# Optimization experiments

Hardware: AMD Instinct MI355X
Metric: run time of the kernel (lower is better)

## Reference

```python
import jax, jax.numpy as jnp
import numpy as np

D_MODEL = 1024
NHEAD = 16
HEAD_DIM = D_MODEL // NHEAD
MASK_FILLER = -1e20


def setup_inputs() -> dict:
    key = jax.random.key(0)
    ks = jax.random.split(key, 8)
    B, S = 2, 2048
    query = jax.random.normal(ks[0], (B, S, D_MODEL), dtype=jnp.float32)
    key_t = jax.random.normal(ks[1], (B, S, D_MODEL), dtype=jnp.float32)
    value = jax.random.normal(ks[2], (B, S, D_MODEL), dtype=jnp.float32)
    mask = jax.random.randint(ks[3], (B, S, S), 0, 2, dtype=jnp.int32)
    # nn.Linear(d_model, d_model, bias=False) weights, shape [out, in]
    scale = 1.0 / np.sqrt(D_MODEL)
    wq = jax.random.uniform(ks[4], (D_MODEL, D_MODEL), jnp.float32, -scale, scale)
    wk = jax.random.uniform(ks[5], (D_MODEL, D_MODEL), jnp.float32, -scale, scale)
    wv = jax.random.uniform(ks[6], (D_MODEL, D_MODEL), jnp.float32, -scale, scale)
    wo = jax.random.uniform(ks[7], (D_MODEL, D_MODEL), jnp.float32, -scale, scale)
    return {"query": query, "key": key_t, "value": value, "mask": mask,
            "wq": wq, "wk": wk, "wv": wv, "wo": wo}


def reference(query, key, value, mask, wq, wk, wv, wo):
    B = query.shape[0]
    # Projections: nn.Linear -> x @ W.T
    q = (query @ wq.T).reshape(B, -1, NHEAD, HEAD_DIM).transpose(0, 2, 1, 3)  # [B,H,Sq,Dh]
    k = (key @ wk.T).reshape(B, -1, NHEAD, HEAD_DIM).transpose(0, 2, 1, 3)    # [B,H,Sk,Dh]
    v = (value @ wv.T).reshape(B, -1, NHEAD, HEAD_DIM).transpose(0, 2, 1, 3)  # [B,H,Sk,Dh]
    scores = jnp.einsum('bhqd,bhkd->bhqk', q, k) / jnp.sqrt(jnp.float32(HEAD_DIM))
    scores = jnp.where(mask[:, None, :, :] == 0, MASK_FILLER, scores)
    attn = jax.nn.softmax(scores, axis=-1)  # dropout p=0.0 -> identity
    out = jnp.einsum('bhqk,bhkd->bhqd', attn, v)  # [B,H,Sq,Dh]
    out = out.transpose(0, 2, 1, 3).reshape(B, -1, D_MODEL)
    return out @ wo.T
```

## Files before the change

kernel.cpp:

```cpp
#include <hip/hip_runtime.h>
#include <stdint.h>

typedef __bf16 bf16x8 __attribute__((ext_vector_type(8)));
typedef __bf16 bf16x4 __attribute__((ext_vector_type(4)));
typedef float floatx4 __attribute__((ext_vector_type(4)));
typedef unsigned short ushort8v __attribute__((ext_vector_type(8)));
typedef unsigned int uint4v __attribute__((ext_vector_type(4)));
typedef unsigned short u16;
typedef unsigned long long u64;

#define GLOAD_LDS16(gp, lp)                                                       \
  __builtin_amdgcn_global_load_lds((__attribute__((address_space(1))) void*)(gp), \
                                   (__attribute__((address_space(3))) void*)(lp), \
                                   16, 0, 0)

__device__ __forceinline__ u16 f2bf(float f) {
  uint32_t u = __builtin_bit_cast(uint32_t, f);
  u = (u + 0x7FFFu + ((u >> 16) & 1u)) >> 16;
  return (u16)u;
}

__device__ __forceinline__ ushort8v load8(const void* base, size_t elemOff, int isf32) {
  if (isf32) {
    const uint32_t* p = (const uint32_t*)base + elemOff;
    uint4v a = *(const uint4v*)p;
    uint4v b = *(const uint4v*)(p + 4);
#pragma unroll
    for (int i = 0; i < 4; ++i) { a[i] += 0x8000u; b[i] += 0x8000u; }
    uint4v r;
    r[0] = __builtin_amdgcn_perm(a[1], a[0], 0x07060302);
    r[1] = __builtin_amdgcn_perm(a[3], a[2], 0x07060302);
    r[2] = __builtin_amdgcn_perm(b[1], b[0], 0x07060302);
    r[3] = __builtin_amdgcn_perm(b[3], b[2], 0x07060302);
    return __builtin_bit_cast(ushort8v, r);
  }
  return *(const ushort8v*)((const u16*)base + elemOff);
}

__global__ void detect_dtype(const u16* __restrict__ q, int* __restrict__ flag) {
  if (threadIdx.x == 0) *flag = 0;
  __syncthreads();
  int hit = 0;
  for (int i = threadIdx.x; i < 8192; i += 256) {
    u16 u = q[i];
    if (((u >> 7) & 0xFF) == 0xFF) hit = 1;
  }
  if (hit) atomicOr(flag, 1);
}

__global__ __launch_bounds__(256)
void prep(const void* X0, const void* X1, const void* X2,
          const void* W0, const void* W1, const void* W2, const void* W3,
          u16* __restrict__ Xb, u16* __restrict__ Wb,
          const int* __restrict__ mask, u64* __restrict__ mpk,
          int* __restrict__ flagOut)
{
  const int id = blockIdx.x;
  const int t  = threadIdx.x;
  if (id < 8192) {
    __shared__ int sflag;
    if (t == 0) sflag = 0;
    int hit = 0;
    {
      const uint4v* q4 = (const uint4v*)X0;
      const int base = t * 4;
#pragma unroll
      for (int i = 0; i < 4; ++i) {
        uint4v v = q4[base + i];
#pragma unroll
        for (int j = 0; j < 4; ++j) {
          const uint32_t w = v[j];
          if ((w & 0x7F80u) == 0x7F80u || (w & 0x7F800000u) == 0x7F800000u)
            hit = 1;
        }
      }
    }
    __syncthreads();
    if (hit) sflag = 1;
    __syncthreads();
    const int isf = sflag;
    if (id == 0 && t == 0) *flagOut = isf;

    const int r2  = t >> 7;
    const int col = (t & 127) * 8;
    const void* src; u16* dst; int row;
    if (id < 6144) {
      const int s = id >> 11;
      src = (s == 0) ? X0 : (s == 1) ? X1 : X2;
      row = (id & 2047) * 2 + r2;
      dst = Xb + (size_t)s * 4096 * 1040 + (size_t)row * 1040 + col;
    } else {
      const int s = (id - 6144) >> 9;
      src = (s == 0) ? W0 : (s == 1) ? W1 : (s == 2) ? W2 : W3;
      row = ((id - 6144) & 511) * 2 + r2;
      dst = Wb + (size_t)s * 1024 * 1040 + (size_t)row * 1040 + col;
    }
    *(ushort8v*)dst = load8(src, (size_t)row * 1024 + col, isf);
  } else {
    const int g    = (id - 8192) * 4 + (t >> 6);
    const int lane = t & 63;
#pragma unroll
    for (int i = 0; i < 4; ++i) {
      const int wordId = g * 4 + i;
      const int row  = wordId >> 5;
      const int word = wordId & 31;
      const int m = mask[(size_t)row * 2048 + word * 64 + lane];
      u64 bits = __ballot(m != 0);
      if (lane == 0) mpk[(size_t)row * 32 + word] = bits;
    }
  }
}

__global__ void pack_mask(const int* __restrict__ mask, u64* __restrict__ mpk) {
  const int gw   = (blockIdx.x * 256 + threadIdx.x) >> 6;
  const int lane = threadIdx.x & 63;
  const int word = gw & 31;
  const int row  = gw >> 5;
  const int m = mask[(size_t)row * 2048 + word * 64 + lane];
  u64 bits = __ballot(m != 0);
  if (lane == 0) mpk[(size_t)row * 32 + word] = bits;
}

__global__ __launch_bounds__(256)
void cvt_w(const void* W0, const void* W1, const void* W2, const void* W3,
           u16* __restrict__ dst, const int* __restrict__ flagp) {
  const int isf = *flagp;
  const int z = blockIdx.y;
  const void* src = (z == 0) ? W0 : (z == 1) ? W1 : (z == 2) ? W2 : W3;
  const size_t off = ((size_t)blockIdx.x * 256 + threadIdx.x) * 8;
  *(ushort8v*)(dst + (size_t)z * 1024 * 1024 + off) = load8(src, off, isf);
}

__global__ __launch_bounds__(256, 3)
void gemm_qkv_b(const u16* __restrict__ Xb, const u16* __restrict__ Wb,
                u16* __restrict__ Qb, u16* __restrict__ Kb, u16* __restrict__ Vt)
{
  const int AS = 1040, WS = 1040, N = 1024, K = 1024;
  const int z = blockIdx.z;
  const u16* A = Xb + (size_t)z * 4096 * AS;
  const u16* W = Wb + (size_t)z * 1024 * WS;

  __shared__ __align__(16) u16 lS[4 * 128 * 32];
  u16* lA = lS;
  u16* lB = lS + 8192;

  const int tid  = threadIdx.x;
  const int lane = tid & 63;
  const int quad = lane >> 4;
  const int l15  = lane & 15;
  const int w    = tid >> 6;
  const int wm   = w >> 1, wn = w & 1;
  const int tileM = blockIdx.x * 128;
  const int tileN = blockIdx.y * 128;

  floatx4 acc[4][4] = {};

  const int ldRow = tid >> 2;
  const int ldCol = (tid & 3) * 8;
  const u16* aG = A + (size_t)(tileM + ldRow) * AS + ldCol;
  const u16* bG = W + (size_t)(tileN + ldRow) * WS + ldCol;
  u16* lAp = lA + tid * 8;
  u16* lBp = lB + tid * 8;

  GLOAD_LDS16(aG, lAp);
  GLOAD_LDS16(aG + (size_t)64 * AS, lAp + 2048);
  GLOAD_LDS16(bG, lBp);
  GLOAD_LDS16(bG + (size_t)64 * WS, lBp + 2048);
  __syncthreads();

#pragma unroll 2
  for (int k0 = 0; k0 < K; k0 += 32) {
    const int cur = (k0 >> 5) & 1;
    const int nxo = 4096 * (cur ^ 1);
    if (k0 + 32 < K) {
      GLOAD_LDS16(aG + k0 + 32, lAp + nxo);
      GLOAD_LDS16(aG + (size_t)64 * AS + k0 + 32, lAp + nxo + 2048);
      GLOAD_LDS16(bG + k0 + 32, lBp + nxo);
      GLOAD_LDS16(bG + (size_t)64 * WS + k0 + 32, lBp + nxo + 2048);
    }
    const u16* cA = lA + 4096 * cur;
    const u16* cB = lB + 4096 * cur;
    bf16x8 af[4], bw[4];
#pragma unroll
    for (int i = 0; i < 4; ++i) {
      af[i] = *(const bf16x8*)&cA[(wm * 64 + i * 16 + l15) * 32 + quad * 8];
      bw[i] = *(const bf16x8*)&cB[(wn * 64 + i * 16 + l15) * 32 + quad * 8];
    }
#pragma unroll
    for (int i = 0; i < 4; ++i)
#pragma unroll
      for (int j = 0; j < 4; ++j)
        acc[i][j] = __builtin_amdgcn_mfma_f32_16x16x32_bf16(af[i], bw[j], acc[i][j], 0, 0, 0);
    __syncthreads();
  }

  if (z < 2) {
    u16* C = (z == 0) ? Qb : Kb;
    const float sc = (z == 0) ? 0.18033688011112042f : 1.0f;
#pragma unroll
    for (int i = 0; i < 4; ++i) {
      const int row0 = tileM + wm * 64 + i * 16 + quad * 4;
#pragma unroll
      for (int j = 0; j < 4; ++j) {
        const int col = tileN + wn * 64 + j * 16 + l15;
#pragma unroll
        for (int r = 0; r < 4; ++r)
          C[(size_t)(row0 + r) * N + col] = f2bf(acc[i][j][r] * sc);
      }
    }
  } else {
    u16* myT = lS + w * 4096;
#pragma unroll
    for (int i = 0; i < 4; ++i)
#pragma unroll
      for (int j = 0; j < 4; ++j)
#pragma unroll
        for (int r = 0; r < 4; ++r) {
          const int lr = i * 16 + quad * 4 + r;
          const int lc = j * 16 + l15;
          myT[lr * 64 + (lc ^ (quad << 4))] = f2bf(acc[i][j][r]);
        }
    {
      const int n    = lane;
      const int gcol = tileN + wn * 64 + n;
      const int hh = gcol >> 6, dd = gcol & 63;
      const int growBase = tileM + wm * 64;
      const int bb = growBase >> 11;
      const int s0 = growBase & 2047;
      u16* dst = Vt + (((size_t)bb * 16 + hh) * 64 + dd) * 2048 + s0;
#pragma unroll
      for (int m0 = 0; m0 < 64; m0 += 8) {
        ushort8v pk;
#pragma unroll
        for (int t = 0; t < 8; ++t) {
          const int m = m0 + t;
          pk[t] = myT[m * 64 + (n ^ ((m & 12) << 2))];
        }
        *(ushort8v*)(dst + m0) = pk;
      }
    }
  }
}

__global__ __launch_bounds__(256)
void gemm_qkv_f(const void* X0, const void* X1, const void* X2,
                const u16* __restrict__ Wb,
                u16* __restrict__ Qb, u16* __restrict__ Kb, u16* __restrict__ Vt,
                const int* __restrict__ flagp)
{
  const int K = 1024, N = 1024;
  const int isf = *flagp;
  const int z = blockIdx.z;
  const void* A_ = (z == 0) ? X0 : (z == 1) ? X1 : X2;
  const u16* W = Wb + (size_t)z * 1024 * 1024;

  __shared__ __align__(16) u16 lA[128 * 32];
  __shared__ __align__(16) u16 lB[128 * 32];

  const int tid  = threadIdx.x;
  const int lane = tid & 63;
  const int quad = lane >> 4;
  const int l15  = lane & 15;
  const int w    = tid >> 6;
  const int wm   = w >> 1, wn = w & 1;
  const int tileM = blockIdx.x * 128;
  const int tileN = blockIdx.y * 128;

  floatx4 acc[4][4] = {};

  const int ldRow = tid >> 2;
  const int ldCol = (tid & 3) * 8;
  const size_t aOff = (size_t)(tileM + ldRow) * K + ldCol;
  const u16* bG = W + (size_t)(tileN + ldRow) * K + ldCol;
  u16* lAp = lA + tid * 8;
  u16* lBp = lB + tid * 8;

  ushort8v a0 = load8(A_, aOff, isf);
  ushort8v a1 = load8(A_, aOff + (size_t)64 * K, isf);
  ushort8v b0 = *(const ushort8v*)bG;
  ushort8v b1 = *(const ushort8v*)(bG + (size_t)64 * K);

  for (int k0 = 0; k0 < K; k0 += 32) {
    __syncthreads();
    *(ushort8v*)lAp          = a0;
    *(ushort8v*)(lAp + 2048) = a1;
    *(ushort8v*)lBp          = b0;
    *(ushort8v*)(lBp + 2048) = b1;
    __syncthreads();

    if (k0 + 32 < K) {
      a0 = load8(A_, aOff + k0 + 32, isf);
      a1 = load8(A_, aOff + (size_t)64 * K + k0 + 32, isf);
      b0 = *(const ushort8v*)(bG + k0 + 32);
      b1 = *(const ushort8v*)(bG + (size_t)64 * K + k0 + 32);
    }

    bf16x8 af[4], bw[4];
#pragma unroll
    for (int i = 0; i < 4; ++i) {
      af[i] = *(const bf16x8*)&lA[(wm * 64 + i * 16 + l15) * 32 + quad * 8];
      bw[i] = *(const bf16x8*)&lB[(wn * 64 + i * 16 + l15) * 32 + quad * 8];
    }
#pragma unroll
    for (int i = 0; i < 4; ++i)
#pragma unroll
      for (int j = 0; j < 4; ++j)
        acc[i][j] = __builtin_amdgcn_mfma_f32_16x16x32_bf16(af[i], bw[j], acc[i][j], 0, 0, 0);
  }

  if (z < 2) {
    u16* C = (z == 0) ? Qb : Kb;
    const float sc = (z == 0) ? 0.18033688011112042f : 1.0f;
#pragma unroll
    for (int i = 0; i < 4; ++i) {
      const int row0 = tileM + wm * 64 + i * 16 + quad * 4;
#pragma unroll
      for (int j = 0; j < 4; ++j) {
        const int col = tileN + wn * 64 + j * 16 + l15;
#pragma unroll
        for (int r = 0; r < 4; ++r)
          C[(size_t)(row0 + r) * N + col] = f2bf(acc[i][j][r] * sc);
      }
    }
  } else {
    const int half = w >> 1;
    u16* myT = (w & 1) ? lB : lA;
#pragma unroll
    for (int pass = 0; pass < 2; ++pass) {
      __syncthreads();
      if (half == pass) {
#pragma unroll
        for (int i = 0; i < 4; ++i)
#pragma unroll
          for (int j = 0; j < 4; ++j)
#pragma unroll
            for (int r = 0; r < 4; ++r) {
              const int lr = i * 16 + quad * 4 + r;
              const int lc = j * 16 + l15;
              myT[lr * 64 + (lc ^ (quad << 4))] = f2bf(acc[i][j][r]);
            }
      }
      __syncthreads();
      if (half == pass) {
        const int n    = lane;
        const int gcol = tileN + wn * 64 + n;
        const int hh = gcol >> 6, dd = gcol & 63;
        const int growBase = tileM + wm * 64;
        const int bb = growBase >> 11;
        const int s0 = growBase & 2047;
        u16* dst = Vt + (((size_t)bb * 16 + hh) * 64 + dd) * 2048 + s0;
#pragma unroll
        for (int m0 = 0; m0 < 64; m0 += 8) {
          ushort8v pk;
#pragma unroll
          for (int t = 0; t < 8; ++t) {
            const int m = m0 + t;
            pk[t] = myT[m * 64 + (n ^ ((m & 12) << 2))];
          }
          *(ushort8v*)(dst + m0) = pk;
        }
      }
    }
  }
}

__global__ __launch_bounds__(256)
void attn(const u16* Qb, const u16* __restrict__ Kb, const u16* __restrict__ Vt,
          const u64* __restrict__ mpk, u16* AO, int aoStr)
{
  __shared__ __align__(16) u16 lK[2][64 * 64];
  __shared__ __align__(16) u16 lV[2][64 * 64];
  __shared__ __align__(16) u16 lP[4][32 * 64];

  const int tid  = threadIdx.x;
  const int lane = tid & 63;
  const int quad = lane >> 4;
  const int l15  = lane & 15;
  const int w    = tid >> 6;

  const int bh = blockIdx.x;
  const int qt = blockIdx.y;
  const int b  = bh >> 4;
  const int h  = bh & 15;
  const size_t rowB   = (size_t)b * 2048;
  const size_t vtBase = ((size_t)bh * 64) * 2048;
  const int qbase = qt * 128 + w * 32;

  bf16x8 aq[2][2];
#pragma unroll
  for (int g = 0; g < 2; ++g) {
    const u16* qp = Qb + (rowB + qbase + g * 16 + l15) * 1024 + h * 64 + quad * 8;
    aq[g][0] = *(const bf16x8*)qp;
    aq[g][1] = *(const bf16x8*)(qp + 32);
  }

  const ushort8v one_u = {0x3F80, 0x3F80, 0x3F80, 0x3F80, 0x3F80, 0x3F80, 0x3F80, 0x3F80};
  const bf16x8 ones = __builtin_bit_cast(bf16x8, one_u);

  floatx4 o[2][4];
  floatx4 l4[2];
#pragma unroll
  for (int g = 0; g < 2; ++g) {
    l4[g] = (floatx4){0.f, 0.f, 0.f, 0.f};
#pragma unroll
    for (int nb = 0; nb < 4; ++nb) o[g][nb] = (floatx4){0.f, 0.f, 0.f, 0.f};
  }

  const u64* mrow0 = mpk + (rowB + qbase + l15) * 32;
  const u64* mrow1 = mpk + (rowB + qbase + 16 + l15) * 32;
  u16* lPw = &lP[w][0];

  const int r1 = tid >> 3;
  const int cs = ((tid & 7) ^ (r1 & 7)) * 8;
  const u16* kSrc = Kb + (rowB + r1) * 1024 + h * 64 + cs;
  const u16* vSrc = Vt + vtBase + (size_t)r1 * 2048 + cs;

  GLOAD_LDS16(kSrc,                     &lK[0][tid * 8]);
  GLOAD_LDS16(kSrc + (size_t)32 * 1024, &lK[0][tid * 8 + 2048]);
  GLOAD_LDS16(vSrc,                     &lV[0][tid * 8]);
  GLOAD_LDS16(vSrc + (size_t)32 * 2048, &lV[0][tid * 8 + 2048]);

#pragma unroll 2
  for (int kt = 0; kt < 32; ++kt) {
    const int cur = kt & 1;
    __syncthreads();
    if (kt < 31) {
      const u16* kS = kSrc + (size_t)(kt + 1) * 64 * 1024;
      const u16* vS = vSrc + (kt + 1) * 64;
      GLOAD_LDS16(kS,                     &lK[cur ^ 1][tid * 8]);
      GLOAD_LDS16(kS + (size_t)32 * 1024, &lK[cur ^ 1][tid * 8 + 2048]);
      GLOAD_LDS16(vS,                     &lV[cur ^ 1][tid * 8]);
      GLOAD_LDS16(vS + (size_t)32 * 2048, &lV[cur ^ 1][tid * 8 + 2048]);
    }

    const u64 mw0 = mrow0[kt];
    const u64 mw1 = mrow1[kt];

#pragma unroll
    for (int nb = 0; nb < 4; ++nb) {
      const int row = nb * 16 + l15;
      const int swk = (row & 7) << 3;
      bf16x8 ak0 = *(const bf16x8*)&lK[cur][row * 64 + ((quad * 8) ^ swk)];
      bf16x8 ak1 = *(const bf16x8*)&lK[cur][row * 64 + ((quad * 8 + 32) ^ swk)];
      floatx4 s0 = {0.f, 0.f, 0.f, 0.f};
      floatx4 s1 = {0.f, 0.f, 0.f, 0.f};
      s0 = __builtin_amdgcn_mfma_f32_16x16x32_bf16(ak0, aq[0][0], s0, 0, 0, 0);
      s1 = __builtin_amdgcn_mfma_f32_16x16x32_bf16(ak0, aq[1][0], s1, 0, 0, 0);
      s0 = __builtin_amdgcn_mfma_f32_16x16x32_bf16(ak1, aq[0][1], s0, 0, 0, 0);
      s1 = __builtin_amdgcn_mfma_f32_16x16x32_bf16(ak1, aq[1][1], s1, 0, 0, 0);
      const int kb = nb * 16 + quad * 4;
      const uint32_t nib0 = (uint32_t)(mw0 >> kb) & 0xFu;
      const uint32_t nib1 = (uint32_t)(mw1 >> kb) & 0xFu;
      const float a0 = (nib0 & 1u) ? __builtin_amdgcn_exp2f(s0[0]) : 0.0f;
      const float a1 = (nib0 & 2u) ? __builtin_amdgcn_exp2f(s0[1]) : 0.0f;
      const float a2 = (nib0 & 4u) ? __builtin_amdgcn_exp2f(s0[2]) : 0.0f;
      const float a3 = (nib0 & 8u) ? __builtin_amdgcn_exp2f(s0[3]) : 0.0f;
      const float c0 = (nib1 & 1u) ? __builtin_amdgcn_exp2f(s1[0]) : 0.0f;
      const float c1 = (nib1 & 2u) ? __builtin_amdgcn_exp2f(s1[1]) : 0.0f;
      const float c2 = (nib1 & 4u) ? __builtin_amdgcn_exp2f(s1[2]) : 0.0f;
      const float c3 = (nib1 & 8u) ? __builtin_amdgcn_exp2f(s1[3]) : 0.0f;
      bf16x4 p0, p1;
      p0[0] = (__bf16)a0; p0[1] = (__bf16)a1;
      p0[2] = (__bf16)a2; p0[3] = (__bf16)a3;
      p1[0] = (__bf16)c0; p1[1] = (__bf16)c1;
      p1[2] = (__bf16)c2; p1[3] = (__bf16)c3;
      const int col = kb ^ ((l15 & 7) << 3);
      *(bf16x4*)&lPw[l15 * 64 + col]        = p0;
      *(bf16x4*)&lPw[(16 + l15) * 64 + col] = p1;
    }

#pragma unroll
    for (int ks = 0; ks < 2; ++ks) {
      const int pc = (ks * 32 + quad * 8) ^ ((l15 & 7) << 3);
      bf16x8 ap0 = *(const bf16x8*)&lPw[l15 * 64 + pc];
      bf16x8 ap1 = *(const bf16x8*)&lPw[(16 + l15) * 64 + pc];
#pragma unroll
      for (int nb = 0; nb < 4; ++nb) {
        const int row = nb * 16 + l15;
        bf16x8 bv = *(const bf16x8*)&lV[cur][row * 64 + ((ks * 32 + quad * 8) ^ ((row & 7) << 3))];
        o[0][nb] = __builtin_amdgcn_mfma_f32_16x16x32_bf16(ap0, bv, o[0][nb], 0, 0, 0);
        o[1][nb] = __builtin_amdgcn_mfma_f32_16x16x32_bf16(ap1, bv, o[1][nb], 0, 0, 0);
      }
      l4[0] = __builtin_amdgcn_mfma_f32_16x16x32_bf16(ap0, ones, l4[0], 0, 0, 0);
      l4[1] = __builtin_amdgcn_mfma_f32_16x16x32_bf16(ap1, ones, l4[1], 0, 0, 0);
    }
  }

#pragma unroll
  for (int g = 0; g < 2; ++g)
#pragma unroll
    for (int r = 0; r < 4; ++r) {
      const float inv = 1.0f / l4[g][r];
      const size_t orow = (rowB + qbase + g * 16 + quad * 4 + r) * aoStr + h * 64;
#pragma unroll
      for (int nb = 0; nb < 4; ++nb)
        AO[orow + nb * 16 + l15] = f2bf(o[g][nb][r] * inv);
    }
}

__global__ __launch_bounds__(256, 4)
void gemm_out(const u16* __restrict__ A, int aStr,
              const u16* __restrict__ W, int wStr, void* C_,
              const int* __restrict__ flagp)
{
  const int K = 1024, N = 1024;
  const int isf = *flagp;

  __shared__ __align__(16) u16 lA[2 * 64 * 32];
  __shared__ __align__(16) u16 lB[2 * 64 * 32];

  const int tid  = threadIdx.x;
  const int lane = tid & 63;
  const int quad = lane >> 4;
  const int l15  = lane & 15;
  const int w    = tid >> 6;
  const int tileM = blockIdx.x * 64;
  const int tileN = blockIdx.y * 64;

  floatx4 acc[4] = {};

  const int ldRow = tid >> 2;
  const int ldCol = (tid & 3) * 8;
  const u16* aG = A + (size_t)(tileM + ldRow) * aStr + ldCol;
  const u16* bG = W + (size_t)(tileN + ldRow) * wStr + ldCol;
  u16* lAp = lA + tid * 8;
  u16* lBp = lB + tid * 8;

  GLOAD_LDS16(aG, lAp);
  GLOAD_LDS16(bG, lBp);
  __syncthreads();

#pragma unroll 2
  for (int k0 = 0; k0 < K; k0 += 32) {
    const int cur = (k0 >> 5) & 1;
    const int nx = 2048 * (cur ^ 1);
    if (k0 + 32 < K) {
      GLOAD_LDS16(aG + k0 + 32, lAp + nx);
      GLOAD_LDS16(bG + k0 + 32, lBp + nx);
    }
    const u16* cA = lA + 2048 * cur;
    const u16* cB = lB + 2048 * cur;
    bf16x8 af[4], bw;
#pragma unroll
    for (int i = 0; i < 4; ++i)
      af[i] = *(const bf16x8*)&cA[(i * 16 + l15) * 32 + quad * 8];
    bw = *(const bf16x8*)&cB[(w * 16 + l15) * 32 + quad * 8];
#pragma unroll
    for (int i = 0; i < 4; ++i)
      acc[i] = __builtin_amdgcn_mfma_f32_16x16x32_bf16(af[i], bw, acc[i], 0, 0, 0);
    __syncthreads();
  }

#pragma unroll
  for (int i = 0; i < 4; ++i) {
    const int row0 = tileM + i * 16 + quad * 4;
    const int col  = tileN + w * 16 + l15;
#pragma unroll
    for (int r = 0; r < 4; ++r) {
      const size_t off = (size_t)(row0 + r) * N + col;
      if (isf) ((float*)C_)[off] = acc[i][r];
      else     ((u16*)C_)[off]   = f2bf(acc[i][r]);
    }
  }
}

extern "C" void kernel_launch(void* const* d_in, const int* in_sizes, int n_in,
                              void* d_out, int out_size, void* d_ws, size_t ws_size,
                              hipStream_t stream)
{
  const int* mk = (const int*)d_in[3];

  int* flag = (int*)d_ws;
  u64* mpk  = (u64*)((char*)d_ws + 256);
  const size_t SZ = (size_t)4096 * 1024;
  u16* Qb = (u16*)((char*)d_ws + 256 + (size_t)1048576);
  u16* Kb = Qb + SZ;
  u16* Vt = Kb + SZ;
  u16* Wb = Vt + SZ;

  const size_t WB_PAD = (size_t)4 * 1024 * 1040;
  const size_t XB_PAD = (size_t)3 * 4096 * 1040;
  const size_t NEED = 256 + 1048576 + 3 * SZ * 2 + WB_PAD * 2 + XB_PAD * 2;

  if (ws_size >= NEED) {
    u16* Xb = Wb + WB_PAD;
    prep<<<16384, 256, 0, stream>>>(d_in[0], d_in[1], d_in[2],
                                    d_in[4], d_in[5], d_in[6], d_in[7],
                                    Xb, Wb, mk, mpk, flag);
    gemm_qkv_b<<<dim3(32, 8, 3), 256, 0, stream>>>(Xb, Wb, Qb, Kb, Vt);
    u16* AOp = Xb;
    attn<<<dim3(32, 16), 256, 0, stream>>>(Qb, Kb, Vt, mpk, AOp, 1040);
    gemm_out<<<dim3(64, 16), 256, 0, stream>>>(AOp, 1040,
                                               Wb + (size_t)3 * 1024 * 1040, 1040,
                                               d_out, flag);
  } else {
    detect_dtype<<<1, 256, 0, stream>>>((const u16*)d_in[0], flag);
    pack_mask<<<32768, 256, 0, stream>>>(mk, mpk);
    cvt_w<<<dim3(512, 4), 256, 0, stream>>>(d_in[4], d_in[5], d_in[6], d_in[7], Wb, flag);
    gemm_qkv_f<<<dim3(32, 8, 3), 256, 0, stream>>>(d_in[0], d_in[1], d_in[2],
                                                   Wb, Qb, Kb, Vt, flag);
    attn<<<dim3(32, 16), 256, 0, stream>>>(Qb, Kb, Vt, mpk, Qb, 1024);
    gemm_out<<<dim3(64, 16), 256, 0, stream>>>(Qb, 1024,
                                               Wb + (size_t)3 * 1024 * 1024, 1024,
                                               d_out, flag);
  }
}
```

Before: 268.5 us.

## Fuse activation bf16 conversion into QKV GEMM A-operand loads

The prep kernel no longer converts the three 4096x1024 activation inputs to padded bf16 buffers. The QKV GEMM instead reads the raw inputs through load8 (converting fp32 to bf16 when needed) into registers one k-step ahead, then stores them to LDS. This removes a full write and re-read of the activation copies. The A operand loses the direct global-to-LDS path, and each activation element is now re-read and re-converted once per N tile.

```diff
diff --git a/kernel.cpp b/kernel.cpp
--- a/kernel.cpp
+++ b/kernel.cpp
@@ -49,15 +49,15 @@
 }
 
 __global__ __launch_bounds__(256)
-void prep(const void* X0, const void* X1, const void* X2,
+void prep(const void* X0,
           const void* W0, const void* W1, const void* W2, const void* W3,
-          u16* __restrict__ Xb, u16* __restrict__ Wb,
+          u16* __restrict__ Wb,
           const int* __restrict__ mask, u64* __restrict__ mpk,
           int* __restrict__ flagOut)
 {
   const int id = blockIdx.x;
   const int t  = threadIdx.x;
-  if (id < 8192) {
+  if (id < 2048) {
     __shared__ int sflag;
     if (t == 0) sflag = 0;
     int hit = 0;
@@ -83,21 +83,13 @@
 
     const int r2  = t >> 7;
     const int col = (t & 127) * 8;
-    const void* src; u16* dst; int row;
-    if (id < 6144) {
-      const int s = id >> 11;
-      src = (s == 0) ? X0 : (s == 1) ? X1 : X2;
-      row = (id & 2047) * 2 + r2;
-      dst = Xb + (size_t)s * 4096 * 1040 + (size_t)row * 1040 + col;
-    } else {
-      const int s = (id - 6144) >> 9;
-      src = (s == 0) ? W0 : (s == 1) ? W1 : (s == 2) ? W2 : W3;
-      row = ((id - 6144) & 511) * 2 + r2;
-      dst = Wb + (size_t)s * 1024 * 1040 + (size_t)row * 1040 + col;
-    }
+    const int s   = id >> 9;
+    const void* src = (s == 0) ? W0 : (s == 1) ? W1 : (s == 2) ? W2 : W3;
+    const int row = (id & 511) * 2 + r2;
+    u16* dst = Wb + (size_t)s * 1024 * 1040 + (size_t)row * 1040 + col;
     *(ushort8v*)dst = load8(src, (size_t)row * 1024 + col, isf);
   } else {
-    const int g    = (id - 8192) * 4 + (t >> 6);
+    const int g    = (id - 2048) * 4 + (t >> 6);
     const int lane = t & 63;
 #pragma unroll
     for (int i = 0; i < 4; ++i) {
@@ -132,13 +124,16 @@
 }
 
 __global__ __launch_bounds__(256, 3)
-void gemm_qkv_b(const u16* __restrict__ Xb, const u16* __restrict__ Wb,
-                u16* __restrict__ Qb, u16* __restrict__ Kb, u16* __restrict__ Vt)
+void gemm_qkv_b(const void* X0, const void* X1, const void* X2,
+                const u16* __restrict__ Wb,
+                u16* __restrict__ Qb, u16* __restrict__ Kb, u16* __restrict__ Vt,
+                const int* __restrict__ flagp)
 {
-  const int AS = 1040, WS = 1040, N = 1024, K = 1024;
+  const int WS = 1040, N = 1024, K = 1024;
   const int z = blockIdx.z;
-  const u16* A = Xb + (size_t)z * 4096 * AS;
+  const void* A_ = (z == 0) ? X0 : (z == 1) ? X1 : X2;
   const u16* W = Wb + (size_t)z * 1024 * WS;
+  const int isf = *flagp;
 
   __shared__ __align__(16) u16 lS[4 * 128 * 32];
   u16* lA = lS;
@@ -157,15 +152,19 @@
 
   const int ldRow = tid >> 2;
   const int ldCol = (tid & 3) * 8;
-  const u16* aG = A + (size_t)(tileM + ldRow) * AS + ldCol;
+  const size_t aOff = (size_t)(tileM + ldRow) * 1024 + ldCol;
   const u16* bG = W + (size_t)(tileN + ldRow) * WS + ldCol;
   u16* lAp = lA + tid * 8;
   u16* lBp = lB + tid * 8;
 
-  GLOAD_LDS16(aG, lAp);
-  GLOAD_LDS16(aG + (size_t)64 * AS, lAp + 2048);
+  ushort8v a0 = load8(A_, aOff, isf);
+  ushort8v a1 = load8(A_, aOff + (size_t)64 * 1024, isf);
+  *(ushort8v*)lAp          = a0;
+  *(ushort8v*)(lAp + 2048) = a1;
   GLOAD_LDS16(bG, lBp);
   GLOAD_LDS16(bG + (size_t)64 * WS, lBp + 2048);
+  a0 = load8(A_, aOff + 32, isf);
+  a1 = load8(A_, aOff + (size_t)64 * 1024 + 32, isf);
   __syncthreads();
 
 #pragma unroll 2
@@ -173,10 +172,14 @@
     const int cur = (k0 >> 5) & 1;
     const int nxo = 4096 * (cur ^ 1);
     if (k0 + 32 < K) {
-      GLOAD_LDS16(aG + k0 + 32, lAp + nxo);
-      GLOAD_LDS16(aG + (size_t)64 * AS + k0 + 32, lAp + nxo + 2048);
+      *(ushort8v*)(lAp + nxo)        = a0;
+      *(ushort8v*)(lAp + nxo + 2048) = a1;
       GLOAD_LDS16(bG + k0 + 32, lBp + nxo);
       GLOAD_LDS16(bG + (size_t)64 * WS + k0 + 32, lBp + nxo + 2048);
+    }
+    if (k0 + 64 < K) {
+      a0 = load8(A_, aOff + k0 + 64, isf);
+      a1 = load8(A_, aOff + (size_t)64 * 1024 + k0 + 64, isf);
     }
     const u16* cA = lA + 4096 * cur;
     const u16* cB = lB + 4096 * cur;
@@ -583,12 +586,12 @@
   const size_t NEED = 256 + 1048576 + 3 * SZ * 2 + WB_PAD * 2 + XB_PAD * 2;
 
   if (ws_size >= NEED) {
-    u16* Xb = Wb + WB_PAD;
-    prep<<<16384, 256, 0, stream>>>(d_in[0], d_in[1], d_in[2],
+    u16* AOp = Wb + WB_PAD;
+    prep<<<10240, 256, 0, stream>>>(d_in[0],
                                     d_in[4], d_in[5], d_in[6], d_in[7],
-                                    Xb, Wb, mk, mpk, flag);
-    gemm_qkv_b<<<dim3(32, 8, 3), 256, 0, stream>>>(Xb, Wb, Qb, Kb, Vt);
-    u16* AOp = Xb;
+                                    Wb, mk, mpk, flag);
+    gemm_qkv_b<<<dim3(32, 8, 3), 256, 0, stream>>>(d_in[0], d_in[1], d_in[2],
+                                                   Wb, Qb, Kb, Vt, flag);
     attn<<<dim3(32, 16), 256, 0, stream>>>(Qb, Kb, Vt, mpk, AOp, 1040);
     gemm_out<<<dim3(64, 16), 256, 0, stream>>>(AOp, 1040,
                                                Wb + (size_t)3 * 1024 * 1040, 1040,
```

After: 290.7 us. +8.3%, slower.
